# Kernel optimization log

Measured on AMD Instinct MI355X. Metric: run time of the kernel, lower is better.

The kernel has to match this reference:

```python
import jax, jax.numpy as jnp
import numpy as np

BN_EPS = 1e-5


def _bn(x, g, b, m, v):
    # inference-mode BatchNorm2d over channel axis 1 of [B,C,F,T]
    scale = (g * jax.lax.rsqrt(v + BN_EPS))[None, :, None, None]
    shift = (b - g * m * jax.lax.rsqrt(v + BN_EPS))[None, :, None, None]
    return x * scale + shift


def _prelu(x, a):
    return jnp.where(x > 0, x, a[None, :, None, None] * x)


def _conv1x1(x, w):
    # w: [out, in]; x: [B,C,F,T]
    return jnp.einsum('oc,bcft->boft', w, x)


def setup_inputs() -> dict:
    key = jax.random.key(0)
    ks = jax.random.split(key, 8)
    B, C, F, T = 4, 64, 256, 400
    d_c = C // 4  # 16
    inp = jax.random.normal(ks[0], (B, C, F, T), dtype=jnp.float32)
    # causal time mask: True = masked (future frames)
    mask = jnp.triu(jnp.ones((T, T), dtype=bool), k=1)[None, None]  # [1,1,T,T]
    w_fqkv = jax.random.normal(ks[1], (3 * d_c, C), dtype=jnp.float32) / np.sqrt(C)
    w_tqk = jax.random.normal(ks[2], (2 * d_c, C), dtype=jnp.float32) / np.sqrt(C)
    w_proj = jax.random.normal(ks[3], (C, d_c), dtype=jnp.float32) / np.sqrt(d_c)
    def bn_params(k, n):
        k1, k2 = jax.random.split(k)
        return (1.0 + 0.1 * jax.random.normal(k1, (n,), dtype=jnp.float32),
                0.1 * jax.random.normal(k2, (n,), dtype=jnp.float32),
                0.1 * jax.random.normal(jax.random.fold_in(k, 7), (n,), dtype=jnp.float32),
                jnp.abs(1.0 + 0.1 * jax.random.normal(jax.random.fold_in(k, 9), (n,), dtype=jnp.float32)))
    g1, b1, m1, v1 = bn_params(ks[4], 3 * d_c)
    g2, b2, m2, v2 = bn_params(ks[5], 2 * d_c)
    g3, b3, m3, v3 = bn_params(ks[6], C)
    a1 = 0.25 * jnp.ones((3 * d_c,), dtype=jnp.float32)
    a2 = 0.25 * jnp.ones((2 * d_c,), dtype=jnp.float32)
    a3 = 0.25 * jnp.ones((C,), dtype=jnp.float32)
    return dict(inp=inp, mask=mask, w_fqkv=w_fqkv, g1=g1, b1=b1, m1=m1, v1=v1, a1=a1,
                w_tqk=w_tqk, g2=g2, b2=b2, m2=m2, v2=v2, a2=a2,
                w_proj=w_proj, g3=g3, b3=b3, m3=m3, v3=v3, a3=a3)


def reference(inp, mask, w_fqkv, g1, b1, m1, v1, a1,
              w_tqk, g2, b2, m2, v2, a2,
              w_proj, g3, b3, m3, v3, a3):
    d_c = w_proj.shape[1]
    scale = 1.0 / np.sqrt(d_c).astype(np.float32)
    # frequency attention
    f_qkv = _prelu(_bn(_conv1x1(inp, w_fqkv), g1, b1, m1, v1), a1)  # [B,3d,F,T]
    qf, kf, v = f_qkv[:, :d_c], f_qkv[:, d_c:2 * d_c], f_qkv[:, 2 * d_c:]
    f_score = jnp.einsum('bcft,bcyt->btfy', qf, kf) * scale
    f_score = jax.nn.softmax(f_score, axis=-1)
    f_out = jnp.einsum('btfy,bcyt->bcft', f_score, v)
    # time attention
    t_qk = _prelu(_bn(_conv1x1(inp, w_tqk), g2, b2, m2, v2), a2)  # [B,2d,F,T]
    qt, kt = t_qk[:, :d_c], t_qk[:, d_c:]
    t_score = jnp.einsum('bcft,bcfy->bfty', qt, kt) * scale
    neg = -jnp.finfo(t_score.dtype).max
    t_score = jnp.where(mask, neg, t_score)
    t_score = jax.nn.softmax(t_score, axis=-1)
    t_out = jnp.einsum('bfty,bcfy->bcft', t_score, f_out)
    out = _prelu(_bn(_conv1x1(t_out, w_proj), g3, b3, m3, v3), a3)
    return out + inp
```

## Files before the change

kernel.cpp:

```cpp
#include <hip/hip_runtime.h>
#include <hip/hip_bf16.h>

#define B_ 4
#define C_ 64
#define F_ 256
#define T_ 400
#define DC 16
#define NB 102400

typedef __hip_bfloat16 bf16;
typedef __attribute__((ext_vector_type(8))) short bf16x8s;
typedef __attribute__((ext_vector_type(4))) short short4v;
typedef __attribute__((ext_vector_type(4))) float f32x4;
typedef __attribute__((ext_vector_type(2))) short short2v;

__device__ __forceinline__ float b2f(bf16 x){ return __bfloat162float(x); }
__device__ __forceinline__ bf16  f2b(float x){ return __float2bfloat16(x); }
__device__ __forceinline__ short f2bs(float x){ bf16 h = __float2bfloat16(x); short s; __builtin_memcpy(&s,&h,2); return s; }

#define MFMA16(a,b,c) __builtin_amdgcn_mfma_f32_16x16x32_bf16((a),(b),(c),0,0,0)

__global__ __launch_bounds__(256) void k_proj(
    const float* __restrict__ inp,
    const float* __restrict__ w_fqkv,
    const float* __restrict__ g1, const float* __restrict__ b1,
    const float* __restrict__ m1, const float* __restrict__ v1,
    const float* __restrict__ a1,
    const float* __restrict__ w_tqk,
    const float* __restrict__ g2, const float* __restrict__ b2,
    const float* __restrict__ m2, const float* __restrict__ v2,
    const float* __restrict__ a2,
    bf16* __restrict__ qf, bf16* __restrict__ kf, bf16* __restrict__ vv,
    bf16* __restrict__ qt, bf16* __restrict__ kt)
{
    __shared__ short Xs[256*64];
    __shared__ short Ws[80*72];
    __shared__ float sc[80], sh[80], al[80];

    const int tid = threadIdx.x;
    const int blk = blockIdx.x;
    const int b   = blk / 400;
    const int rem = blk - b*400;
    const int f0  = (rem & 15) * 16;
    const int t0  = (rem >> 4) * 16;

    for (int i = tid; i < 80*32; i += 256) {
        int o = i >> 5, cp = (i & 31) * 2;
        const float* src = (o < 48) ? &w_fqkv[o*64 + cp] : &w_tqk[(o-48)*64 + cp];
        short2v wv; wv.x = f2bs(src[0]); wv.y = f2bs(src[1]);
        *(short2v*)&Ws[o*72 + cp] = wv;
    }
    if (tid < 48) {
        float rs = rsqrtf(v1[tid] + 1e-5f);
        float g  = g1[tid];
        sc[tid] = g * rs;
        sh[tid] = b1[tid] - g * m1[tid] * rs;
        al[tid] = a1[tid];
    }
    if (tid >= 128 && tid < 160) {
        int o = tid - 128;
        float rs = rsqrtf(v2[o] + 1e-5f);
        float g  = g2[o];
        sc[48+o] = g * rs;
        sh[48+o] = b2[o] - g * m2[o] * rs;
        al[48+o] = a2[o];
    }

    {
        const int wv = tid >> 6, lnn = tid & 63;
        const int fi = lnn >> 2, tc = lnn & 3;
        const float* xb = inp + (size_t)b*64*NB + (size_t)(f0+fi)*T_ + t0 + tc*4;
        #pragma unroll
        for (int p = 0; p < 16; p++) {
            const int c = p*4 + wv;
            f32x4 x = *(const f32x4*)&xb[(size_t)c*NB];
            const int chi = c >> 3, clo = c & 7;
            #pragma unroll
            for (int j = 0; j < 4; j++) {
                int r = (tc*4 + j)*16 + fi;
                int slot = chi ^ (r & 7) ^ ((r >> 4) & 7);
                Xs[r*64 + slot*8 + clo] = f2bs(x[j]);
            }
        }
    }
    __syncthreads();

    const int wave = tid >> 6;
    const int lane = tid & 63;
    const int ln   = lane & 15;
    const int quad = lane >> 4;
    const f32x4 zero = {0.f,0.f,0.f,0.f};

    bf16x8s B1[4][2];
    bf16x8s B2[4][2];
    #pragma unroll
    for (int nt = 0; nt < 4; nt++) {
        const int tile = wave*4 + nt;
        {
            const int r  = tile*16 + ln;
            const int sw = (ln & 7) ^ (tile & 7);
            B1[nt][0] = *(const bf16x8s*)&Xs[r*64 + ((quad     ^ sw) * 8)];
            B1[nt][1] = *(const bf16x8s*)&Xs[r*64 + (((4+quad) ^ sw) * 8)];
        }
        {
            const int r  = ln*16 + tile;
            const int sw = (tile & 7) ^ (ln & 7);
            B2[nt][0] = *(const bf16x8s*)&Xs[r*64 + ((quad     ^ sw) * 8)];
            B2[nt][1] = *(const bf16x8s*)&Xs[r*64 + (((4+quad) ^ sw) * 8)];
        }
    }

    #pragma unroll
    for (int mt = 0; mt < 5; mt++) {
        bf16x8s A0 = *(const bf16x8s*)&Ws[(mt*16+ln)*72 + quad*8];
        bf16x8s A1 = *(const bf16x8s*)&Ws[(mt*16+ln)*72 + 32 + quad*8];
        float scv[4], shv[4], alv[4];
        #pragma unroll
        for (int r = 0; r < 4; r++) {
            int o = mt*16 + quad*4 + r;
            scv[r] = sc[o]; shv[r] = sh[o]; alv[r] = al[o];
        }
        #pragma unroll
        for (int nt = 0; nt < 4; nt++) {
            bf16x8s Bb0 = (mt < 3) ? B1[nt][0] : B2[nt][0];
            bf16x8s Bb1 = (mt < 3) ? B1[nt][1] : B2[nt][1];
            f32x4 acc = MFMA16(A0, Bb0, zero);
            acc = MFMA16(A1, Bb1, acc);
            short4v hs;
            #pragma unroll
            for (int r = 0; r < 4; r++) {
                float y = acc[r]*scv[r] + shv[r];
                y = y > 0.f ? y : alv[r]*y;
                if (mt == 0 || mt == 3) y *= 0.25f;
                hs[r] = f2bs(y);
            }
            const int tile = wave*4 + nt;
            if (mt < 3) {
                size_t idx = (((size_t)b*T_ + (t0+tile))*F_ + (f0+ln))*DC + quad*4;
                bf16* dst = (mt == 0) ? qf : (mt == 1) ? kf : vv;
                *(short4v*)((short*)dst + idx) = hs;
            } else {
                size_t idx = (((size_t)b*F_ + (f0+tile))*T_ + (t0+ln))*DC + quad*4;
                bf16* dst = (mt == 3) ? qt : kt;
                *(short4v*)((short*)dst + idx) = hs;
            }
        }
    }
}

__global__ __launch_bounds__(256) void k_fattn(
    const bf16* __restrict__ qf, const bf16* __restrict__ kf,
    const bf16* __restrict__ vv, bf16* __restrict__ fout)
{
    __shared__ short Ks[F_*24];
    __shared__ short Vt[16*264];
    __shared__ short Pb[4][16*72];

    const int bt = blockIdx.x;
    const int b = bt / T_, t = bt - b*T_;
    const size_t base = ((size_t)b*T_ + t)*F_*DC;
    const short* kfp = (const short*)(kf + base);
    const short* vvp = (const short*)(vv + base);
    const short* qfp = (const short*)(qf + base);
    const int tid = threadIdx.x;

    for (int i = tid; i < F_*8; i += 256) {
        int r = i >> 3, cp = (i & 7) * 2;
        short2v v = *(const short2v*)&kfp[r*16+cp];
        *(short2v*)&Ks[r*24+cp] = v;
    }
    for (int i = tid; i < F_*8; i += 256) {
        int f = i >> 3, cp = (i & 7) * 2;
        short2v v = *(const short2v*)&vvp[f*16+cp];
        Vt[cp*264 + f]     = v.x;
        Vt[(cp+1)*264 + f] = v.y;
    }
    __syncthreads();

    const int wave = tid >> 6;
    const int lane = tid & 63;
    const int ln   = lane & 15;
    const int quad = lane >> 4;
    short* Pw = &Pb[wave][0];
    const f32x4 zero = {0.f,0.f,0.f,0.f};

    for (int s = wave; s < F_/16; s += 4) {
        bf16x8s A = {};
        if (quad < 2) A = *(const bf16x8s*)&qfp[(s*16+ln)*16 + quad*8];

        f32x4 sum = zero, O = zero;
        for (int ch = 0; ch < 4; ch++) {
            #pragma unroll
            for (int i2 = 0; i2 < 4; i2++) {
                int yt = ch*4 + i2;
                bf16x8s Bf = {};
                if (quad < 2) Bf = *(const bf16x8s*)&Ks[(yt*16+ln)*24 + quad*8];
                f32x4 S = MFMA16(A, Bf, zero);
                #pragma unroll
                for (int r = 0; r < 4; r++) {
                    float p = __expf(S[r]);
                    sum[r] += p;
                    Pw[(quad*4+r)*72 + i2*16 + ln] = f2bs(p);
                }
            }
            #pragma unroll
            for (int h = 0; h < 2; h++) {
                bf16x8s Pa = *(const bf16x8s*)&Pw[ln*72 + h*32 + quad*8];
                bf16x8s Vb = *(const bf16x8s*)&Vt[ln*264 + ch*64 + h*32 + quad*8];
                O = MFMA16(Pa, Vb, O);
            }
        }
        #pragma unroll
        for (int m = 1; m < 16; m <<= 1) {
            #pragma unroll
            for (int r = 0; r < 4; r++) sum[r] += __shfl_xor(sum[r], m, 64);
        }
        #pragma unroll
        for (int r = 0; r < 4; r++) {
            int f = s*16 + quad*4 + r;
            fout[(((size_t)b*F_ + f)*T_ + t)*DC + ln] = f2b(O[r]/sum[r]);
        }
    }
}

__global__ __launch_bounds__(256) void k_tattn(
    const bf16* __restrict__ qt, const bf16* __restrict__ kt,
    const bf16* __restrict__ fo, bf16* __restrict__ tout)
{
    __shared__ short Ks[T_*24];
    __shared__ short Vt[16*456];
    __shared__ short Pb[4][16*72];

    const int bfi = blockIdx.x;
    const int b = bfi / F_, f = bfi - b*F_;
    const size_t base = ((size_t)b*F_ + f)*T_*DC;
    const short* ktp = (const short*)(kt + base);
    const short* fop = (const short*)(fo + base);
    const short* qtp = (const short*)(qt + base);
    const int tid = threadIdx.x;

    for (int i = tid; i < T_*8; i += 256) {
        int r = i >> 3, cp = (i & 7) * 2;
        short2v v = *(const short2v*)&ktp[r*16+cp];
        *(short2v*)&Ks[r*24+cp] = v;
    }
    for (int i = tid; i < T_*8; i += 256) {
        int y = i >> 3, cp = (i & 7) * 2;
        short2v v = *(const short2v*)&fop[y*16+cp];
        Vt[cp*456 + y]     = v.x;
        Vt[(cp+1)*456 + y] = v.y;
    }
    for (int i = tid; i < 16*64; i += 256) {
        int c = i >> 6, y = T_ + (i & 63);
        if (y < 456) Vt[c*456 + y] = 0;
    }
    __syncthreads();

    const int wave = tid >> 6;
    const int lane = tid & 63;
    const int ln   = lane & 15;
    const int quad = lane >> 4;
    short* Pw = &Pb[wave][0];
    const f32x4 zero = {0.f,0.f,0.f,0.f};

    for (int s = wave; s < 25; s += 4) {
        bf16x8s A = {};
        if (quad < 2) A = *(const bf16x8s*)&qtp[(s*16+ln)*16 + quad*8];

        f32x4 sum = zero, O = zero;
        const int nch = (s + 4) >> 2;
        for (int ch = 0; ch < nch; ch++) {
            #pragma unroll
            for (int i2 = 0; i2 < 4; i2++) {
                int yt = ch*4 + i2;
                if (yt <= s) {
                    bf16x8s Bf = {};
                    if (quad < 2) Bf = *(const bf16x8s*)&Ks[(yt*16+ln)*24 + quad*8];
                    f32x4 S = MFMA16(A, Bf, zero);
                    const bool diag = (yt == s);
                    #pragma unroll
                    for (int r = 0; r < 4; r++) {
                        float p = __expf(S[r]);
                        if (diag && ln > quad*4+r) p = 0.f;
                        sum[r] += p;
                        Pw[(quad*4+r)*72 + i2*16 + ln] = f2bs(p);
                    }
                } else {
                    #pragma unroll
                    for (int r = 0; r < 4; r++)
                        Pw[(quad*4+r)*72 + i2*16 + ln] = 0;
                }
            }
            #pragma unroll
            for (int h = 0; h < 2; h++) {
                bf16x8s Pa = *(const bf16x8s*)&Pw[ln*72 + h*32 + quad*8];
                bf16x8s Vb = *(const bf16x8s*)&Vt[ln*456 + ch*64 + h*32 + quad*8];
                O = MFMA16(Pa, Vb, O);
            }
        }
        #pragma unroll
        for (int m = 1; m < 16; m <<= 1) {
            #pragma unroll
            for (int r = 0; r < 4; r++) sum[r] += __shfl_xor(sum[r], m, 64);
        }
        #pragma unroll
        for (int r = 0; r < 4; r++) {
            int t = s*16 + quad*4 + r;
            tout[base + (size_t)t*DC + ln] = f2b(O[r]/sum[r]);
        }
    }
}

__global__ __launch_bounds__(256) void k_proj2(
    const bf16* __restrict__ tog, const float* __restrict__ w_proj,
    const float* __restrict__ g3, const float* __restrict__ b3,
    const float* __restrict__ m3, const float* __restrict__ v3,
    const float* __restrict__ a3,
    const float* __restrict__ inp, float* __restrict__ out)
{
    __shared__ short Ws2[64*24];
    __shared__ float sc[64], sh[64], al[64];

    const int tid = threadIdx.x;
    const int b   = blockIdx.x / 400;
    const int n0  = (blockIdx.x - b*400) * 256;

    for (int i = tid; i < 64*8; i += 256) {
        int o = i >> 3, cp = (i & 7) * 2;
        short2v wv; wv.x = f2bs(w_proj[o*16+cp]); wv.y = f2bs(w_proj[o*16+cp+1]);
        *(short2v*)&Ws2[o*24 + cp] = wv;
    }
    if (tid < 64) {
        float rs = rsqrtf(v3[tid] + 1e-5f);
        float g  = g3[tid];
        sc[tid] = g * rs;
        sh[tid] = b3[tid] - g * m3[tid] * rs;
        al[tid] = a3[tid];
    }
    __syncthreads();

    const int wave = tid >> 6;
    const int lane = tid & 63;
    const int ln   = lane & 15;
    const int quad = lane >> 4;
    const f32x4 zero = {0.f,0.f,0.f,0.f};
    const short* top = (const short*)tog + (size_t)b*NB*DC;

    bf16x8s Bf[4];
    #pragma unroll
    for (int nt = 0; nt < 4; nt++) {
        Bf[nt] = (bf16x8s){};
        if (quad < 2) {
            int n = n0 + wave*64 + nt*16 + ln;
            Bf[nt] = *(const bf16x8s*)&top[(size_t)n*DC + quad*8];
        }
    }

    #pragma unroll
    for (int mt = 0; mt < 4; mt++) {
        bf16x8s A = {};
        if (quad < 2) A = *(const bf16x8s*)&Ws2[(mt*16+ln)*24 + quad*8];
        float scv[4], shv[4], alv[4];
        #pragma unroll
        for (int r = 0; r < 4; r++) {
            int o = mt*16 + quad*4 + r;
            scv[r] = sc[o]; shv[r] = sh[o]; alv[r] = al[o];
        }
        #pragma unroll
        for (int nt = 0; nt < 4; nt++) {
            f32x4 acc = MFMA16(A, Bf[nt], zero);
            const int n = n0 + wave*64 + nt*16 + ln;
            #pragma unroll
            for (int r = 0; r < 4; r++) {
                int o = mt*16 + quad*4 + r;
                float y = acc[r]*scv[r] + shv[r];
                y = y > 0.f ? y : alv[r]*y;
                size_t gi = ((size_t)b*64 + o)*NB + n;
                out[gi] = y + inp[gi];
            }
        }
    }
}

extern "C" void kernel_launch(void* const* d_in, const int* in_sizes, int n_in,
                              void* d_out, int out_size, void* d_ws, size_t ws_size,
                              hipStream_t stream)
{
    const float* inp    = (const float*)d_in[0];
    const float* w_fqkv = (const float*)d_in[2];
    const float* g1 = (const float*)d_in[3],  *b1 = (const float*)d_in[4];
    const float* m1 = (const float*)d_in[5],  *v1 = (const float*)d_in[6];
    const float* a1 = (const float*)d_in[7];
    const float* w_tqk  = (const float*)d_in[8];
    const float* g2 = (const float*)d_in[9],  *b2 = (const float*)d_in[10];
    const float* m2 = (const float*)d_in[11], *v2 = (const float*)d_in[12];
    const float* a2 = (const float*)d_in[13];
    const float* w_proj = (const float*)d_in[14];
    const float* g3 = (const float*)d_in[15], *b3 = (const float*)d_in[16];
    const float* m3 = (const float*)d_in[17], *v3 = (const float*)d_in[18];
    const float* a3 = (const float*)d_in[19];
    float* out = (float*)d_out;

    const size_t NQ = (size_t)B_*T_*F_*DC;
    bf16* ws = (bf16*)d_ws;
    bf16 *qf = ws,        *kf = ws + NQ,   *vv = ws + 2*NQ;
    bf16 *qt = ws + 3*NQ, *kt = ws + 4*NQ;
    bf16 *fo = ws + 5*NQ, *to = ws + 6*NQ;

    k_proj <<<B_*400, 256, 0, stream>>>(inp, w_fqkv, g1,b1,m1,v1,a1,
                                        w_tqk, g2,b2,m2,v2,a2,
                                        qf, kf, vv, qt, kt);
    k_fattn<<<B_*T_, 256, 0, stream>>>(qf, kf, vv, fo);
    k_tattn<<<B_*F_, 256, 0, stream>>>(qt, kt, fo, to);
    k_proj2<<<B_*400, 256, 0, stream>>>(to, w_proj, g3,b3,m3,v3,a3, inp, out);
}
```

Measured before the change: 376.5 us.

## Keep attention probabilities in registers via transposed MFMA and permlane swaps

Both attention kernels now compute S transposed (K as the A operand) so the exp'd probabilities can be packed to bf16 with v_cvt_pk_bf16 and rearranged with permlane32/16 swaps straight into the second MFMA operand. This removes the per-wave LDS round trip for P. The row-sum reduction shrinks to two shuffles, a reciprocal replaces the division, and outputs are written as vectorized 8-byte stores. K/V staging uses 16-byte loads. The time-attention kernel also uses a hand-balanced static schedule of causal row tiles across the four waves, which introduces lane-layout correctness risk.

```diff
diff --git a/kernel.cpp b/kernel.cpp
--- a/kernel.cpp
+++ b/kernel.cpp
@@ -13,12 +13,26 @@
 typedef __attribute__((ext_vector_type(4))) short short4v;
 typedef __attribute__((ext_vector_type(4))) float f32x4;
 typedef __attribute__((ext_vector_type(2))) short short2v;
+typedef __attribute__((ext_vector_type(2))) unsigned int uint2v;
+typedef __attribute__((ext_vector_type(4))) unsigned int uint4v;
 
 __device__ __forceinline__ float b2f(bf16 x){ return __bfloat162float(x); }
 __device__ __forceinline__ bf16  f2b(float x){ return __float2bfloat16(x); }
 __device__ __forceinline__ short f2bs(float x){ bf16 h = __float2bfloat16(x); short s; __builtin_memcpy(&s,&h,2); return s; }
 
 #define MFMA16(a,b,c) __builtin_amdgcn_mfma_f32_16x16x32_bf16((a),(b),(c),0,0,0)
+
+__device__ __forceinline__ unsigned cvt_pk_bf16(float a, float b){
+    unsigned r;
+    asm("v_cvt_pk_bf16_f32 %0, %1, %2" : "=v"(r) : "v"(a), "v"(b));
+    return r;
+}
+__device__ __forceinline__ void permlane32_swap(unsigned &a, unsigned &b){
+    asm("v_permlane32_swap_b32 %0, %1" : "+v"(a), "+v"(b));
+}
+__device__ __forceinline__ void permlane16_swap(unsigned &a, unsigned &b){
+    asm("v_permlane16_swap_b32 %0, %1" : "+v"(a), "+v"(b));
+}
 
 __global__ __launch_bounds__(256) void k_proj(
     const float* __restrict__ inp,
@@ -65,7 +79,6 @@
         sh[48+o] = b2[o] - g * m2[o] * rs;
         al[48+o] = a2[o];
     }
-
     {
         const int wv = tid >> 6, lnn = tid & 63;
         const int fi = lnn >> 2, tc = lnn & 3;
@@ -154,7 +167,6 @@
 {
     __shared__ short Ks[F_*24];
     __shared__ short Vt[16*264];
-    __shared__ short Pb[4][16*72];
 
     const int bt = blockIdx.x;
     const int b = bt / T_, t = bt - b*T_;
@@ -164,16 +176,17 @@
     const short* qfp = (const short*)(qf + base);
     const int tid = threadIdx.x;
 
-    for (int i = tid; i < F_*8; i += 256) {
-        int r = i >> 3, cp = (i & 7) * 2;
-        short2v v = *(const short2v*)&kfp[r*16+cp];
-        *(short2v*)&Ks[r*24+cp] = v;
-    }
-    for (int i = tid; i < F_*8; i += 256) {
-        int f = i >> 3, cp = (i & 7) * 2;
-        short2v v = *(const short2v*)&vvp[f*16+cp];
-        Vt[cp*264 + f]     = v.x;
-        Vt[(cp+1)*264 + f] = v.y;
+    for (int i = tid; i < F_*2; i += 256) {
+        int r = i >> 1, cp = (i & 1) * 8;
+        *(bf16x8s*)&Ks[r*24+cp] = *(const bf16x8s*)&kfp[r*16+cp];
+    }
+    for (int i = tid; i < F_; i += 256) {
+        bf16x8s v0 = *(const bf16x8s*)&vvp[i*16];
+        bf16x8s v1 = *(const bf16x8s*)&vvp[i*16+8];
+        #pragma unroll
+        for (int c = 0; c < 8; c++) Vt[c*264 + i]     = v0[c];
+        #pragma unroll
+        for (int c = 0; c < 8; c++) Vt[(8+c)*264 + i] = v1[c];
     }
     __syncthreads();
 
@@ -181,45 +194,50 @@
     const int lane = tid & 63;
     const int ln   = lane & 15;
     const int quad = lane >> 4;
-    short* Pw = &Pb[wave][0];
     const f32x4 zero = {0.f,0.f,0.f,0.f};
 
     for (int s = wave; s < F_/16; s += 4) {
-        bf16x8s A = {};
-        if (quad < 2) A = *(const bf16x8s*)&qfp[(s*16+ln)*16 + quad*8];
-
-        f32x4 sum = zero, O = zero;
+        bf16x8s Qf = {};
+        if (quad < 2) Qf = *(const bf16x8s*)&qfp[(s*16+ln)*16 + quad*8];
+
+        float ssum = 0.f;
+        f32x4 O = zero;
         for (int ch = 0; ch < 4; ch++) {
+            unsigned w[4][2];
             #pragma unroll
             for (int i2 = 0; i2 < 4; i2++) {
                 int yt = ch*4 + i2;
-                bf16x8s Bf = {};
-                if (quad < 2) Bf = *(const bf16x8s*)&Ks[(yt*16+ln)*24 + quad*8];
-                f32x4 S = MFMA16(A, Bf, zero);
+                bf16x8s Kf = {};
+                if (quad < 2) Kf = *(const bf16x8s*)&Ks[(yt*16+ln)*24 + quad*8];
+                f32x4 S = MFMA16(Kf, Qf, zero);
+                f32x4 p;
                 #pragma unroll
-                for (int r = 0; r < 4; r++) {
-                    float p = __expf(S[r]);
-                    sum[r] += p;
-                    Pw[(quad*4+r)*72 + i2*16 + ln] = f2bs(p);
-                }
+                for (int r = 0; r < 4; r++) { p[r] = __expf(S[r]); ssum += p[r]; }
+                w[i2][0] = cvt_pk_bf16(p[0], p[1]);
+                w[i2][1] = cvt_pk_bf16(p[2], p[3]);
             }
             #pragma unroll
             for (int h = 0; h < 2; h++) {
-                bf16x8s Pa = *(const bf16x8s*)&Pw[ln*72 + h*32 + quad*8];
+                unsigned t0a = w[2*h][0],   t0b = w[2*h][1];
+                unsigned t1a = w[2*h+1][0], t1b = w[2*h+1][1];
+                permlane32_swap(t0a, t1a);
+                permlane32_swap(t0b, t1b);
+                permlane16_swap(t0a, t1a);
+                permlane16_swap(t0b, t1b);
+                union { uint4v u; bf16x8s v; } P;
+                P.u = (uint4v){t0a, t0b, t1a, t1b};
                 bf16x8s Vb = *(const bf16x8s*)&Vt[ln*264 + ch*64 + h*32 + quad*8];
-                O = MFMA16(Pa, Vb, O);
-            }
-        }
-        #pragma unroll
-        for (int m = 1; m < 16; m <<= 1) {
-            #pragma unroll
-            for (int r = 0; r < 4; r++) sum[r] += __shfl_xor(sum[r], m, 64);
-        }
-        #pragma unroll
-        for (int r = 0; r < 4; r++) {
-            int f = s*16 + quad*4 + r;
-            fout[(((size_t)b*F_ + f)*T_ + t)*DC + ln] = f2b(O[r]/sum[r]);
-        }
+                O = MFMA16(Vb, P.v, O);
+            }
+        }
+        ssum += __shfl_xor(ssum, 16, 64);
+        ssum += __shfl_xor(ssum, 32, 64);
+        float rinv = __builtin_amdgcn_rcpf(ssum);
+        unsigned o0 = cvt_pk_bf16(O[0]*rinv, O[1]*rinv);
+        unsigned o1 = cvt_pk_bf16(O[2]*rinv, O[3]*rinv);
+        const int f = s*16 + ln;
+        *(uint2v*)((short*)fout + (((size_t)b*F_ + f)*T_ + t)*DC + quad*4)
+            = (uint2v){o0, o1};
     }
 }
 
@@ -229,7 +247,6 @@
 {
     __shared__ short Ks[T_*24];
     __shared__ short Vt[16*456];
-    __shared__ short Pb[4][16*72];
 
     const int bfi = blockIdx.x;
     const int b = bfi / F_, f = bfi - b*F_;
@@ -239,16 +256,17 @@
     const short* qtp = (const short*)(qt + base);
     const int tid = threadIdx.x;
 
-    for (int i = tid; i < T_*8; i += 256) {
-        int r = i >> 3, cp = (i & 7) * 2;
-        short2v v = *(const short2v*)&ktp[r*16+cp];
-        *(short2v*)&Ks[r*24+cp] = v;
-    }
-    for (int i = tid; i < T_*8; i += 256) {
-        int y = i >> 3, cp = (i & 7) * 2;
-        short2v v = *(const short2v*)&fop[y*16+cp];
-        Vt[cp*456 + y]     = v.x;
-        Vt[(cp+1)*456 + y] = v.y;
+    for (int i = tid; i < T_*2; i += 256) {
+        int r = i >> 1, cp = (i & 1) * 8;
+        *(bf16x8s*)&Ks[r*24+cp] = *(const bf16x8s*)&ktp[r*16+cp];
+    }
+    for (int i = tid; i < T_; i += 256) {
+        bf16x8s v0 = *(const bf16x8s*)&fop[i*16];
+        bf16x8s v1 = *(const bf16x8s*)&fop[i*16+8];
+        #pragma unroll
+        for (int c = 0; c < 8; c++) Vt[c*456 + i]     = v0[c];
+        #pragma unroll
+        for (int c = 0; c < 8; c++) Vt[(8+c)*456 + i] = v1[c];
     }
     for (int i = tid; i < 16*64; i += 256) {
         int c = i >> 6, y = T_ + (i & 63);
@@ -260,54 +278,70 @@
     const int lane = tid & 63;
     const int ln   = lane & 15;
     const int quad = lane >> 4;
-    short* Pw = &Pb[wave][0];
     const f32x4 zero = {0.f,0.f,0.f,0.f};
 
-    for (int s = wave; s < 25; s += 4) {
-        bf16x8s A = {};
-        if (quad < 2) A = *(const bf16x8s*)&qtp[(s*16+ln)*16 + quad*8];
-
-        f32x4 sum = zero, O = zero;
-        const int nch = (s + 4) >> 2;
+    unsigned long long sched;
+    switch (wave) {
+      case 0:  sched = 24ull | (16ull<<5) | (12ull<<10) | ( 8ull<<15) | ( 4ull<<20) | ( 0ull<<25) | ( 3ull<<30); break;
+      case 1:  sched = 23ull | (19ull<<5) | (15ull<<10) | (11ull<<15) | ( 7ull<<20) | ( 2ull<<25) | ( 1ull<<30); break;
+      case 2:  sched = 22ull | (18ull<<5) | (14ull<<10) | (10ull<<15) | ( 9ull<<20) | ( 5ull<<25) | (31ull<<30); break;
+      default: sched = 21ull | (17ull<<5) | (13ull<<10) | (20ull<<15) | ( 6ull<<20) | (31ull<<25) | (31ull<<30); break;
+    }
+
+    for (int it = 0; it < 7; it++) {
+        const int s = (int)((sched >> (5*it)) & 31);
+        if (s == 31) break;
+
+        bf16x8s Qf = {};
+        if (quad < 2) Qf = *(const bf16x8s*)&qtp[(s*16+ln)*16 + quad*8];
+
+        float ssum = 0.f;
+        f32x4 O = zero;
+        const int nch = (s >> 2) + 1;
         for (int ch = 0; ch < nch; ch++) {
+            unsigned w[4][2];
             #pragma unroll
             for (int i2 = 0; i2 < 4; i2++) {
                 int yt = ch*4 + i2;
                 if (yt <= s) {
-                    bf16x8s Bf = {};
-                    if (quad < 2) Bf = *(const bf16x8s*)&Ks[(yt*16+ln)*24 + quad*8];
-                    f32x4 S = MFMA16(A, Bf, zero);
+                    bf16x8s Kf = {};
+                    if (quad < 2) Kf = *(const bf16x8s*)&Ks[(yt*16+ln)*24 + quad*8];
+                    f32x4 S = MFMA16(Kf, Qf, zero);
                     const bool diag = (yt == s);
+                    f32x4 p;
                     #pragma unroll
                     for (int r = 0; r < 4; r++) {
-                        float p = __expf(S[r]);
-                        if (diag && ln > quad*4+r) p = 0.f;
-                        sum[r] += p;
-                        Pw[(quad*4+r)*72 + i2*16 + ln] = f2bs(p);
+                        p[r] = __expf(S[r]);
+                        if (diag && (quad*4 + r > ln)) p[r] = 0.f;
+                        ssum += p[r];
                     }
+                    w[i2][0] = cvt_pk_bf16(p[0], p[1]);
+                    w[i2][1] = cvt_pk_bf16(p[2], p[3]);
                 } else {
-                    #pragma unroll
-                    for (int r = 0; r < 4; r++)
-                        Pw[(quad*4+r)*72 + i2*16 + ln] = 0;
+                    w[i2][0] = 0u; w[i2][1] = 0u;
                 }
             }
             #pragma unroll
             for (int h = 0; h < 2; h++) {
-                bf16x8s Pa = *(const bf16x8s*)&Pw[ln*72 + h*32 + quad*8];
+                unsigned t0a = w[2*h][0],   t0b = w[2*h][1];
+                unsigned t1a = w[2*h+1][0], t1b = w[2*h+1][1];
+                permlane32_swap(t0a, t1a);
+                permlane32_swap(t0b, t1b);
+                permlane16_swap(t0a, t1a);
+                permlane16_swap(t0b, t1b);
+                union { uint4v u; bf16x8s v; } P;
+                P.u = (uint4v){t0a, t0b, t1a, t1b};
                 bf16x8s Vb = *(const bf16x8s*)&Vt[ln*456 + ch*64 + h*32 + quad*8];
-                O = MFMA16(Pa, Vb, O);
-            }
-        }
-        #pragma unroll
-        for (int m = 1; m < 16; m <<= 1) {
-            #pragma unroll
-            for (int r = 0; r < 4; r++) sum[r] += __shfl_xor(sum[r], m, 64);
-        }
-        #pragma unroll
-        for (int r = 0; r < 4; r++) {
-            int t = s*16 + quad*4 + r;
-            tout[base + (size_t)t*DC + ln] = f2b(O[r]/sum[r]);
-        }
+                O = MFMA16(Vb, P.v, O);
+            }
+        }
+        ssum += __shfl_xor(ssum, 16, 64);
+        ssum += __shfl_xor(ssum, 32, 64);
+        float rinv = __builtin_amdgcn_rcpf(ssum);
+        unsigned o0 = cvt_pk_bf16(O[0]*rinv, O[1]*rinv);
+        unsigned o1 = cvt_pk_bf16(O[2]*rinv, O[3]*rinv);
+        *(uint2v*)((short*)tout + base + (size_t)(s*16+ln)*DC + quad*4)
+            = (uint2v){o0, o1};
     }
 }
 
```

New measurement: 342.5 us. -9.0%, faster.
